# Optimization experiments

Hardware: AMD Instinct MI355X
Metric: run time of the kernel (lower is better)

The kernel has to match this reference:

```python
import jax, jax.numpy as jnp
import numpy as np
from jax import lax

B, INC1, INC2, H, W = 8, 64, 128, 128, 128
EPS = 1e-5  # BatchNorm eps; inference mode with running_mean=0, running_var=1


def leaky(x):
    return jnp.where(x >= 0, x, 0.01 * x)


def conv2d(x, w, pad=0, dil=1, groups=1):
    return lax.conv_general_dilated(
        x, w, (1, 1), [(pad, pad), (pad, pad)], rhs_dilation=(dil, dil),
        dimension_numbers=('NCHW', 'OIHW', 'NCHW'), feature_group_count=groups)


def bnlrelu(x, g, b):
    s = g / jnp.sqrt(1.0 + EPS)
    return leaky(x * s[None, :, None, None] + b[None, :, None, None])


def interp_bilinear_ac(x, oh, ow):
    # bilinear, align_corners=True (matches F.interpolate)
    ih, iw = x.shape[-2], x.shape[-1]
    ys = jnp.linspace(0.0, ih - 1.0, oh)
    xs = jnp.linspace(0.0, iw - 1.0, ow)
    y0 = jnp.floor(ys).astype(jnp.int32); y1 = jnp.minimum(y0 + 1, ih - 1)
    x0 = jnp.floor(xs).astype(jnp.int32); x1 = jnp.minimum(x0 + 1, iw - 1)
    wy = (ys - y0)[:, None]; wx = xs - x0
    rows = x[..., y0, :] * (1.0 - wy) + x[..., y1, :] * wy
    return rows[..., x0] * (1.0 - wx) + rows[..., x1] * wx


def se_layer(x, w1, w2):
    y = x.mean(axis=(2, 3))                     # [B, C]
    y = jax.nn.sigmoid(leaky(y @ w1.T) @ w2.T)  # squeeze-excite gates
    return x * y[:, :, None, None]


def dyn_multidil(f2, k):
    # per-sample depthwise conv with input-dependent 5x5 kernels, 3 dilations
    C = k.shape[1]
    def per_sample(fi, ki):
        xi = fi[None]            # [1, C, H, W]
        wi = ki[:, None, :, :]   # [C, 1, 5, 5]
        r = conv2d(xi, wi, pad=2, dil=1, groups=C)
        r = r + conv2d(xi, wi, pad=4, dil=2, groups=C)
        r = r + conv2d(xi, wi, pad=6, dil=3, groups=C)
        return r[0]
    out = jax.vmap(per_sample)(f2, k)
    return out.at[0].set(f2[0])  # original python loop starts at i=1: sample 0 untouched


def _forward(x1, k, conv1_w, conv1_g, conv1_b, conv2_w, conv2_g, conv2_b,
             conv_w, conv_bias, c0_w, c0_g, c0_b, attc_w, attc_g, attc_b,
             c05_w, c05_g, c05_b, conv0a_w, conv0a_g, conv0a_b,
             conv0b_w, conv0b_g, conv0b_b, se_w1, se_w2):
    h, w = x1.shape[2], x1.shape[3]
    kse = interp_bilinear_ac(k, h, w)                       # [B, inc1, H, W]
    va = x1.mean(axis=(2, 3), keepdims=True)                # AdaptiveAvgPool2d(1)
    bias = conv_bias[None, :, None, None]
    # MaxPool2d(1) is identity, so conv(vm) == conv(x1); bias added in both terms
    fuseadd = (conv2d(va, conv_w) + bias) + (conv2d(x1, conv_w) + bias)
    fuseadd = fuseadd * kse + fuseadd
    att = jax.nn.sigmoid(fuseadd)
    eadd = bnlrelu(conv2d(fuseadd, c0_w, pad=1), c0_g, c0_b)
    A1 = jax.nn.sigmoid(bnlrelu(conv2d(eadd, attc_w, pad=1), attc_g, attc_b))
    att = se_layer(att, se_w1, se_w2)
    f1 = bnlrelu(conv2d(x1, conv1_w), conv1_g, conv1_b)
    f2 = bnlrelu(conv2d(x1, conv2_w), conv2_g, conv2_b)
    out1 = bnlrelu(conv2d(f1, c0_w, pad=1), c0_g, c0_b)
    out1 = out1 * kse + out1
    A2 = jax.nn.sigmoid(bnlrelu(conv2d(out1, attc_w, pad=1), attc_g, attc_b))
    out2 = dyn_multidil(f2, k)
    out2 = out2 * kse + out2
    out2conv = bnlrelu(conv2d(out2, c05_w, pad=2), c05_g, c05_b)
    fuseout2 = A1 * A2 * out2conv
    finout2 = bnlrelu(conv2d(fuseout2, c05_w, pad=2), c05_g, c05_b)
    eout2 = finout2 + out2conv + f2
    out2 = bnlrelu(conv2d(eout2, c05_w, pad=2), c05_g, c05_b)
    out = jnp.concatenate([out1, out2], axis=1)             # [B, 2*inc1, H, W]
    out = bnlrelu(conv2d(out, conv0a_w), conv0a_g, conv0a_b)
    out = bnlrelu(conv2d(out, conv0b_w, pad=1), conv0b_g, conv0b_b)
    return att * out * A1


def setup_inputs() -> dict:
    key = jax.random.key(0)
    ks = jax.random.split(key, 32)
    f32 = jnp.float32
    def w(i, shape, s=0.05):
        return jax.random.normal(ks[i], shape, f32) * s
    return {
        'x1': jax.random.normal(ks[0], (B, INC2, H, W), f32),
        'k': jax.random.normal(ks[1], (B, INC1, 5, 5), f32) * 0.2,
        'conv1_w': w(2, (INC1, INC2, 1, 1)),
        'conv1_g': 1.0 + w(3, (INC1,)),
        'conv1_b': w(4, (INC1,)),
        'conv2_w': w(5, (INC1, INC2, 1, 1)),
        'conv2_g': 1.0 + w(6, (INC1,)),
        'conv2_b': w(7, (INC1,)),
        'conv_w': w(8, (INC1, INC2, 1, 1)),
        'conv_bias': w(9, (INC1,)),
        'c0_w': w(10, (INC1, INC1, 3, 3)),
        'c0_g': 1.0 + w(11, (INC1,)),
        'c0_b': w(12, (INC1,)),
        'attc_w': w(13, (INC1, INC1, 3, 3)),
        'attc_g': 1.0 + w(14, (INC1,)),
        'attc_b': w(15, (INC1,)),
        'c05_w': w(16, (INC1, INC1, 5, 5)),
        'c05_g': 1.0 + w(17, (INC1,)),
        'c05_b': w(18, (INC1,)),
        'conv0a_w': w(19, (INC1, 2 * INC1, 1, 1)),
        'conv0a_g': 1.0 + w(20, (INC1,)),
        'conv0a_b': w(21, (INC1,)),
        'conv0b_w': w(22, (INC1, INC1, 3, 3)),
        'conv0b_g': 1.0 + w(23, (INC1,)),
        'conv0b_b': w(24, (INC1,)),
        'se_w1': w(25, (INC1 // 16, INC1)),
        'se_w2': w(26, (INC1, INC1 // 16)),
    }


def reference(x1, k, conv1_w, conv1_g, conv1_b, conv2_w, conv2_g, conv2_b,
              conv_w, conv_bias, c0_w, c0_g, c0_b, attc_w, attc_g, attc_b,
              c05_w, c05_g, c05_b, conv0a_w, conv0a_g, conv0a_b,
              conv0b_w, conv0b_g, conv0b_b, se_w1, se_w2):
    return _forward(x1, k, conv1_w, conv1_g, conv1_b, conv2_w, conv2_g, conv2_b,
                    conv_w, conv_bias, c0_w, c0_g, c0_b, attc_w, attc_g, attc_b,
                    c05_w, c05_g, c05_b, conv0a_w, conv0a_g, conv0a_b,
                    conv0b_w, conv0b_g, conv0b_b, se_w1, se_w2)
```

## Files before the change

kernel.cpp:

```cpp
#include <hip/hip_runtime.h>
#include <math.h>

#define HW 16384
#define EPSC 1.00001f

typedef short bf16x8 __attribute__((ext_vector_type(8)));
typedef float f32x4 __attribute__((ext_vector_type(4)));
typedef float f32x16 __attribute__((ext_vector_type(16)));

static __device__ __forceinline__ unsigned short f2bf(float f) {
    unsigned int u = __float_as_uint(f);
    unsigned int r = (u + 0x7fffu + ((u >> 16) & 1u)) >> 16;
    return (unsigned short)r;
}
static __device__ __forceinline__ float bf2f(unsigned short u) {
    return __uint_as_float(((unsigned int)u) << 16);
}

__global__ void mean_hw_kernel(const float* __restrict__ x, float* __restrict__ out) {
    int blk = blockIdx.x;
    const float4* p4 = (const float4*)(x + (size_t)blk * HW);
    float s = 0.f;
    for (int i = threadIdx.x; i < HW / 4; i += 256) {
        float4 v = p4[i];
        s += v.x + v.y + v.z + v.w;
    }
    for (int off = 32; off > 0; off >>= 1) s += __shfl_down(s, off, 64);
    __shared__ float red[4];
    int lane = threadIdx.x & 63, wid = threadIdx.x >> 6;
    if (lane == 0) red[wid] = s;
    __syncthreads();
    if (threadIdx.x == 0)
// ... 72 lines not shown
        const float* src = x1 + ((size_t)b * 128 + h * 64) * HW + p0;
        __syncthreads();
        for (int e = threadIdx.x; e < 4096; e += 256) {
            int ci = e >> 6, px = e & 63;
            t[ci][px] = src[(size_t)ci * HW + px];
        }
        __syncthreads();
        unsigned short* dst = (h == 0 ? xa : xb) + ((size_t)b * HW + p0) * 64;
        for (int e = threadIdx.x; e < 4096; e += 256) {
            int px = e >> 6, ci = e & 63;
            dst[(size_t)px * 64 + ci] = f2bf(t[ci][px]);
        }
    }
}

__global__ void prep_w_kernel(const float* __restrict__ src, unsigned short* __restrict__ dst,
                              int CO, int CI, int K, int co_total, int co_off) {
    int idx = blockIdx.x * 256 + threadIdx.x;
    int total = CO * CI * K * K;
    if (idx >= total) return;
    int kx = idx % K, t1 = idx / K;
    int ky = t1 % K, t2 = t1 / K;
    int ci = t2 % CI, co = t2 / CI;
    int tap = ky * K + kx, chunk = ci >> 5, k32 = ci & 31;
    int kc = tap * (CI >> 5) + chunk;
    dst[((size_t)kc * co_total + co_off + co) * 32 + k32] = f2bf(src[idx]);
}

__global__ void prep_w32_kernel(const float* __restrict__ src, unsigned short* __restrict__ dst,
                                int CO, int CI, int K) {
    int idx = blockIdx.x * 256 + threadIdx.x;
    int total = CO * CI * K * K;
    if (idx >= total) return;
    int kx = idx % K, t1 = idx / K;
    int ky = t1 % K, t2 = t1 / K;
    int ci = t2 % CI, co = t2 / CI;
    int tap = ky * K + kx;
    int kstep = ci >> 4, khalf = (ci >> 3) & 1, j = ci & 7;
    int l = khalf * 32 + (co & 31), mb = co >> 5;
    dst[(((size_t)(tap * 4 + kstep) * 2 + mb) * 64 + l) * 8 + j] = f2bf(src[idx]);
}

__global__ void prep_w16_kernel(const float* __restrict__ src, unsigned short* __restrict__ dst,
                                int CO, int CI) {
    int idx = blockIdx.x * 256 + threadIdx.x;
    if (idx >= CO * CI) return;
    int ci = idx % CI, co = idx / CI;
    int ch = ci >> 5, q = (ci >> 3) & 3, j = ci & 7;
    int l = q * 16 + (co & 15), mb = co >> 4;
    dst[(((size_t)ch * 4 + mb) * 64 + l) * 8 + j] = f2bf(src[idx]);
}

template<int KSZ>
__global__ __launch_bounds__(256, 2) void conv_mfma32(
    const unsigned short* __restrict__ Xa,
    const unsigned short* __restrict__ Wp,
    const float* __restrict__ g, const float* __restrict__ bb,
    const float* __restrict__ kk,
    const unsigned short* __restrict__ eB, const unsigned short* __restrict__ eC,
    unsigned short* __restrict__ out_bf, unsigned short* __restrict__ aux_bf, int emode)
{
    constexpr int PAD = KSZ / 2;
    constexpr int TWX = 16 + 2 * PAD;
    constexpr int TWY = 16 + 2 * PAD;
    constexpr int NTAP = KSZ * KSZ;
    constexpr int WSLAB = 4 * 2 * 64 * 8;
    __shared__ unsigned short xs[TWY * TWX * 64];
    __shared__ unsigned short ws[2 * WSLAB];

    const int b = blockIdx.y;
    const int ty = (blockIdx.x >> 3) * 16, tx = (blockIdx.x & 7) * 16;
    const int tid = threadIdx.x;
    const int lane = tid & 63, wv = tid >> 6;
    const int n32 = lane & 31, khalf = lane >> 5;

    int rr[2], cc2[2];
#pragma unroll
    for (int nt = 0; nt < 2; ++nt) {
        int p = wv * 64 + nt * 32 + n32;
        rr[nt] = p >> 4; cc2[nt] = p & 15;
    }

    uint4 wst[2];
    {
        const uint4* gw = (const uint4*)Wp;
#pragma unroll
        for (int s = 0; s < 2; ++s) wst[s] = gw[tid + s * 256];
    }
    for (int e = tid; e < TWY * TWX * 8; e += 256) {
        int ci8 = e & 7, pxl = e >> 3;
        int xx = pxl % TWX, yy = pxl / TWX;
        int gy = ty + yy - PAD, gx = tx + xx - PAD;
        uint4 v = {0u, 0u, 0u, 0u};
        if (gy >= 0 && gy < 128 && gx >= 0 && gx < 128)
            v = *(const uint4*)(Xa + (((size_t)b * HW + gy * 128 + gx) * 64 + ci8 * 8));
        *(uint4*)(&xs[(size_t)pxl * 64 + ((ci8 ^ (pxl & 7)) << 3)]) = v;
    }
    {
        uint4* lw = (uint4*)ws;
#pragma unroll
        for (int s = 0; s < 2; ++s) lw[tid + s * 256] = wst[s];
    }
    __syncthreads();

    f32x16 acc[2][2];
#pragma unroll
    for (int mb = 0; mb < 2; ++mb)
#pragma unroll
        for (int nt = 0; nt < 2; ++nt)
#pragma unroll
            for (int i = 0; i < 16; ++i) acc[mb][nt][i] = 0.f;

    for (int tap = 0; tap < NTAP; ++tap) {
        if (tap + 1 < NTAP) {
            const uint4* gw = (const uint4*)Wp + (size_t)(tap + 1) * (WSLAB / 8);
#pragma unroll
            for (int s = 0; s < 2; ++s) wst[s] = gw[tid + s * 256];
        }
        const unsigned short* wl = ws + (tap & 1) * WSLAB;
        const int ky = tap / KSZ, kx = tap - ky * KSZ;
        int pxl0 = (rr[0] + ky) * TWX + cc2[0] + kx;
        int pxl1 = (rr[1] + ky) * TWX + cc2[1] + kx;
        int sw0 = (pxl0 & 7), sw1 = (pxl1 & 7);
#pragma unroll
        for (int kstep = 0; kstep < 4; ++kstep) {
            bf16x8 af0 = *(const bf16x8*)(wl + ((kstep * 2 + 0) * 64 + lane) * 8);
            bf16x8 af1 = *(const bf16x8*)(wl + ((kstep * 2 + 1) * 64 + lane) * 8);
            int gidx = kstep * 2 + khalf;
            bf16x8 b0 = *(const bf16x8*)(&xs[(size_t)pxl0 * 64 + ((gidx ^ sw0) << 3)]);
            bf16x8 b1 = *(const bf16x8*)(&xs[(size_t)pxl1 * 64 + ((gidx ^ sw1) << 3)]);
            acc[0][0] = __builtin_amdgcn_mfma_f32_32x32x16_bf16(af0, b0, acc[0][0], 0, 0, 0);
            acc[0][1] = __builtin_amdgcn_mfma_f32_32x32x16_bf16(af0, b1, acc[0][1], 0, 0, 0);
            acc[1][0] = __builtin_amdgcn_mfma_f32_32x32x16_bf16(af1, b0, acc[1][0], 0, 0, 0);
            acc[1][1] = __builtin_amdgcn_mfma_f32_32x32x16_bf16(af1, b1, acc[1][1], 0, 0, 0);
        }
        if (tap + 1 < NTAP) {
            uint4* lw = (uint4*)(ws + ((tap + 1) & 1) * WSLAB);
#pragma unroll
            for (int s = 0; s < 2; ++s) lw[tid + s * 256] = wst[s];
            __syncthreads();
        }
    }

    const float rs = rsqrtf(EPSC);
#pragma unroll
    for (int mb = 0; mb < 2; ++mb) {
#pragma unroll
        for (int nt = 0; nt < 2; ++nt) {
            const int py = ty + rr[nt];
            const int px = tx + cc2[nt];
            const size_t pix = (size_t)b * HW + py * 128 + px;
#pragma unroll
            for (int rq = 0; rq < 4; ++rq) {
                const int co0 = mb * 32 + rq * 8 + khalf * 4;
                float v4[4];
#pragma unroll
                for (int rg = 0; rg < 4; ++rg) {
                    int co = co0 + rg;
                    float v = acc[mb][nt][rq * 4 + rg];
                    v = fmaf(v, g[co] * rs, bb[co]);
                    v = v >= 0.f ? v : 0.01f * v;
                    if (emode == 1 || emode == 6) v = 1.0f / (1.0f + __expf(-v));
                    else if (emode == 2)
                        v *= (1.0f + kse_val(kk + (size_t)(b * 64 + co) * 25, py, px));
                    v4[rg] = v;
                }
                if (emode == 6) {
                    ushort4 e = *(const ushort4*)(eB + pix * 64 + co0);
                    *(ushort4*)(out_bf + pix * 64 + co0) = (ushort4){
                        f2bf(v4[0] * bf2f(e.x)), f2bf(v4[1] * bf2f(e.y)),
                        f2bf(v4[2] * bf2f(e.z)), f2bf(v4[3] * bf2f(e.w))};
                } else if (emode == 4) {
                    *(ushort4*)(out_bf + pix * 64 + co0) =
                        (ushort4){f2bf(v4[0]), f2bf(v4[1]), f2bf(v4[2]), f2bf(v4[3])};
                    ushort4 e = *(const ushort4*)(eB + pix * 64 + co0);
                    *(ushort4*)(aux_bf + pix * 64 + co0) = (ushort4){
                        f2bf(v4[0] * bf2f(e.x)), f2bf(v4[1] * bf2f(e.y)),
                        f2bf(v4[2] * bf2f(e.z)), f2bf(v4[3] * bf2f(e.w))};
                } else if (emode == 5) {
                    ushort4 e1 = *(const ushort4*)(eB + pix * 64 + co0);
                    ushort4 e2 = *(const ushort4*)(eC + pix * 64 + co0);
                    *(ushort4*)(out_bf + pix * 64 + co0) = (ushort4){
                        f2bf(v4[0] + bf2f(e1.x) + bf2f(e2.x)),
                        f2bf(v4[1] + bf2f(e1.y) + bf2f(e2.y)),
                        f2bf(v4[2] + bf2f(e1.z) + bf2f(e2.z)),
                        f2bf(v4[3] + bf2f(e1.w) + bf2f(e2.w))};
                } else {
                    *(ushort4*)(out_bf + pix * 64 + co0) =
                        (ushort4){f2bf(v4[0]), f2bf(v4[1]), f2bf(v4[2]), f2bf(v4[3])};
                }
            }
        }
    }
}

__global__ __launch_bounds__(256, 2) void conv_mfma1x1(
    const unsigned short* __restrict__ Xa, const unsigned short* __restrict__ Xb,
    const unsigned short* __restrict__ Wp,
    const float* __restrict__ g, const float* __restrict__ bb,
    unsigned short* __restrict__ out_bf)
{
    constexpr int CI = 128;
    __shared__ unsigned short xs[128 * CI];
    __shared__ unsigned short ws[4 * 4 * 64 * 8];
    const int b = blockIdx.y;
    const int ty = (blockIdx.x >> 3) * 8, tx = (blockIdx.x & 7) * 16;
    const int tid = threadIdx.x;
    const int lane = tid & 63, wv = tid >> 6;
    const int n = lane & 15, quad = lane >> 4;

    {
// ... 26 lines not shown
        for (int nt = 0; nt < 2; ++nt) {
            int pxl = (r0 + nt) * 16 + n;
            bfr[nt] = *(const bf16x8*)(&xs[(size_t)pxl * CI +
                                           (((ch * 4 + quad) ^ (pxl & 7)) << 3)]);
        }
#pragma unroll
        for (int mb = 0; mb < 4; ++mb) {
            bf16x8 af = *(const bf16x8*)(ws + ((ch * 4 + mb) * 64 + lane) * 8);
#pragma unroll
            for (int nt = 0; nt < 2; ++nt)
                acc[mb][nt] = __builtin_amdgcn_mfma_f32_16x16x32_bf16(
                    af, bfr[nt], acc[mb][nt], 0, 0, 0);
        }
    }

    const float rs = rsqrtf(EPSC);
#pragma unroll
    for (int mb = 0; mb < 4; ++mb) {
#pragma unroll
        for (int nt = 0; nt < 2; ++nt) {
            const int py = ty + r0 + nt, px = tx + n;
            const size_t pix = (size_t)b * HW + py * 128 + px;
            const int co0 = mb * 16 + quad * 4;
            float v4[4];
#pragma unroll
            for (int rg = 0; rg < 4; ++rg) {
                float v = fmaf(acc[mb][nt][rg], g[co0 + rg] * rs, bb[co0 + rg]);
                v4[rg] = v >= 0.f ? v : 0.01f * v;
            }
            *(ushort4*)(out_bf + pix * 64 + co0) =
                (ushort4){f2bf(v4[0]), f2bf(v4[1]), f2bf(v4[2]), f2bf(v4[3])};
        }
    }
}

__global__ __launch_bounds__(256, 2) void conv1x1_triple(
    const unsigned short* __restrict__ Xa, const unsigned short* __restrict__ Xb,
    const unsigned short* __restrict__ Wp,
    const float* __restrict__ cva, const float* __restrict__ cbias,
    const float* __restrict__ g1, const float* __restrict__ b1,
    const float* __restrict__ g2, const float* __restrict__ b2,
    const float* __restrict__ kk,
    unsigned short* __restrict__ fuse_bf, unsigned short* __restrict__ att0_bf,
    unsigned short* __restrict__ f1_bf,
    float* __restrict__ f2_f32, unsigned short* __restrict__ f2_bf)
{
    constexpr int CI = 128;
    __shared__ unsigned short xs[128 * CI];
    __shared__ unsigned short ws[4 * 192 * 32];
    const int b = blockIdx.y;
    const int ty = (blockIdx.x >> 3) * 8, tx = (blockIdx.x & 7) * 16;
    const int tid = threadIdx.x;
    const int lane = tid & 63, wv = tid >> 6;
    const int n = lane & 15, quad = lane >> 4;

    {
        const uint4* gw = (const uint4*)Wp;
        uint4* lw = (uint4*)ws;
#pragma unroll
        for (int s = 0; s < 12; ++s) lw[tid + s * 256] = gw[tid + s * 256];
    }
    for (int e = tid; e < 128 * 16; e += 256) {
        int ci8 = e & 15, pxl = e >> 4;
        int gy = ty + (pxl >> 4), gx = tx + (pxl & 15);
        const unsigned short* src = (ci8 >= 8) ? Xb : Xa;
        int c8 = ci8 & 7;
        uint4 v = *(const uint4*)(src + (((size_t)b * HW + gy * 128 + gx) * 64 + c8 * 8));
        *(uint4*)(&xs[(size_t)pxl * CI + ((ci8 ^ (pxl & 7)) << 3)]) = v;
    }
    __syncthreads();

    f32x4 acc[12][2];
#pragma unroll
    for (int mb = 0; mb < 12; ++mb)
#pragma unroll
        for (int nt = 0; nt < 2; ++nt) acc[mb][nt] = (f32x4){0.f, 0.f, 0.f, 0.f};

    const int r0 = wv * 2;
#pragma unroll
    for (int ch = 0; ch < 4; ++ch) {
        bf16x8 bfr[2];
#pragma unroll
        for (int nt = 0; nt < 2; ++nt) {
            int pxl = (r0 + nt) * 16 + n;
            bfr[nt] = *(const bf16x8*)(&xs[(size_t)pxl * CI +
                                           (((ch * 4 + quad) ^ (pxl & 7)) << 3)]);
        }
#pragma unroll
        for (int mb = 0; mb < 12; ++mb) {
            bf16x8 af = *(const bf16x8*)(ws + (ch * 192 + mb * 16 + n) * 32 + quad * 8);
#pragma unroll
            for (int nt = 0; nt < 2; ++nt)
                acc[mb][nt] = __builtin_amdgcn_mfma_f32_16x16x32_bf16(
                    af, bfr[nt], acc[mb][nt], 0, 0, 0);
        }
    }

    const float rs = rsqrtf(EPSC);
#pragma unroll
    for (int mb = 0; mb < 12; ++mb) {
#pragma unroll
        for (int nt = 0; nt < 2; ++nt) {
            const int py = ty + r0 + nt;
            const int px = tx + n;
            const size_t pix = (size_t)b * HW + py * 128 + px;
            const int cg = mb * 16 + quad * 4;
            if (mb < 4) {
                float v4[4], s4[4];
#pragma unroll
                for (int rg = 0; rg < 4; ++rg) {
                    int co = cg + rg;
                    float base = cva[b * 64 + co] + 2.0f * cbias[co];
                    float fa = (acc[mb][nt][rg] + base) *
                               (1.0f + kse_val(kk + (size_t)(b * 64 + co) * 25, py, px));
                    v4[rg] = fa;
                    s4[rg] = 1.0f / (1.0f + __expf(-fa));
                }
                *(ushort4*)(fuse_bf + pix * 64 + cg) =
                    (ushort4){f2bf(v4[0]), f2bf(v4[1]), f2bf(v4[2]), f2bf(v4[3])};
                *(ushort4*)(att0_bf + pix * 64 + cg) =
                    (ushort4){f2bf(s4[0]), f2bf(s4[1]), f2bf(s4[2]), f2bf(s4[3])};
            } else if (mb < 8) {
                int co0 = cg - 64;
                float v4[4];
#pragma unroll
                for (int rg = 0; rg < 4; ++rg) {
                    float v = fmaf(acc[mb][nt][rg], g1[co0 + rg] * rs, b1[co0 + rg]);
                    v4[rg] = v >= 0.f ? v : 0.01f * v;
                }
                *(ushort4*)(f1_bf + pix * 64 + co0) =
                    (ushort4){f2bf(v4[0]), f2bf(v4[1]), f2bf(v4[2]), f2bf(v4[3])};
            } else {
                int co0 = cg - 128;
                float v4[4];
#pragma unroll
                for (int rg = 0; rg < 4; ++rg) {
                    float v = fmaf(acc[mb][nt][rg], g2[co0 + rg] * rs, b2[co0 + rg]);
                    v4[rg] = v >= 0.f ? v : 0.01f * v;
                    f2_f32[(size_t)(b * 64 + co0 + rg) * HW + py * 128 + px] = v4[rg];
                }
                *(ushort4*)(f2_bf + pix * 64 + co0) =
                    (ushort4){f2bf(v4[0]), f2bf(v4[1]), f2bf(v4[2]), f2bf(v4[3])};
            }
        }
    }
}

__global__ __launch_bounds__(256) void dyndil_kernel(const float* __restrict__ f2,
                                                     const float* __restrict__ kk,
                                                     unsigned short* __restrict__ out2bf) {
    __shared__ float xl[44][148];
    int b = blockIdx.x >> 8, c = (blockIdx.x >> 2) & 63, band = blockIdx.x & 3;
    int y0 = band * 32;
    int tid = threadIdx.x;
    int r = tid >> 3, s = tid & 7;
    int x0 = s * 16;
    int y = y0 + r;
    const float* xp = f2 + (size_t)(b * 64 + c) * HW;
    const float* kt = kk + (size_t)(b * 64 + c) * 25;
    float acc[16];

    if (b != 0) {
        for (int e = tid; e < 44 * 148; e += 256) {
            int rr = e / 148, cc = e - rr * 148;
            int yy = y0 + rr - 6, xx = cc - 8;
// ... 39 lines not shown
#pragma unroll
        for (int i = 0; i < 4; i++) {
            float4 v = p4[i];
            acc[i*4] = v.x; acc[i*4+1] = v.y; acc[i*4+2] = v.z; acc[i*4+3] = v.w;
        }
    }
    float ys = y * (4.0f / 127.0f);
    int yi0 = (int)ys; if (yi0 > 4) yi0 = 4;
    int yi1 = yi0 + 1; if (yi1 > 4) yi1 = 4;
    float wy = ys - (float)yi0;
    float ry0 = kt[yi0*5+0] * (1.f-wy) + kt[yi1*5+0] * wy;
    float ry1 = kt[yi0*5+1] * (1.f-wy) + kt[yi1*5+1] * wy;
    float ry2 = kt[yi0*5+2] * (1.f-wy) + kt[yi1*5+2] * wy;
    float ry3 = kt[yi0*5+3] * (1.f-wy) + kt[yi1*5+3] * wy;
    float ry4 = kt[yi0*5+4] * (1.f-wy) + kt[yi1*5+4] * wy;
    unsigned short* op = out2bf + ((size_t)b * HW + (size_t)y * 128 + x0) * 64 + c;
#pragma unroll
    for (int e = 0; e < 16; e++) {
        int x = x0 + e;
        float xs2 = x * (4.0f / 127.0f);
        int xi0 = (int)xs2; if (xi0 > 4) xi0 = 4;
        float wx = xs2 - (float)xi0;
        float a = xi0==0 ? ry0 : xi0==1 ? ry1 : xi0==2 ? ry2 : xi0==3 ? ry3 : ry4;
        float bs = xi0>=3 ? ry4 : (xi0==2 ? ry3 : (xi0==1 ? ry2 : ry1));
        float kv = a + (bs - a) * wx;
        op[(size_t)e * 64] = f2bf(acc[e] * (1.0f + kv));
    }
}

__global__ void final_kernel(const unsigned short* __restrict__ att0,
                             const float* __restrict__ scale,
                             const unsigned short* __restrict__ outb,
                             const unsigned short* __restrict__ a1,
                             float* __restrict__ o) {
    __shared__ float t[64][65];
    int b = blockIdx.y;
    int p0 = blockIdx.x * 64;
    int tid = threadIdx.x;
    for (int e = tid; e < 4096; e += 256) {
        int px = e >> 6, c = e & 63;
        size_t idx = ((size_t)b * HW + p0 + px) * 64 + c;
// ... 38 lines not shown
    const float* se_w2 = (const float*)d_in[26];

    const size_t U = (size_t)8 * HW * 64 * 2;
    unsigned char* P = (unsigned char*)d_ws;
    unsigned short* x1a        = (unsigned short*)(P + 0 * U);
    unsigned short* x1b        = (unsigned short*)(P + 1 * U);
    unsigned short* att0_bf    = (unsigned short*)(P + 2 * U);
    unsigned short* fuse_bf    = (unsigned short*)(P + 3 * U);
    unsigned short* f1_bf      = (unsigned short*)(P + 4 * U);
    float*          f2         = (float*)         (P + 5 * U);
    unsigned short* f2_bf      = (unsigned short*)(P + 7 * U);
    unsigned short* A1_bf      = (unsigned short*)(P + 8 * U);
    unsigned short* eadd_bf    = (unsigned short*)(P + 9 * U);
    unsigned short* out1_bf    = (unsigned short*)(P + 10 * U);
    unsigned short* A12_bf     = (unsigned short*)(P + 11 * U);
    unsigned short* out2_bf     = x1a;
    unsigned short* oc_bf       = x1b;
    unsigned short* fuseout2_bf = fuse_bf;
    unsigned short* eout2_bf    = f1_bf;
    unsigned short* out2fin_bf  = eadd_bf;
    unsigned short* outb_bf     = out1_bf;
    unsigned short* outa_bf     = A12_bf;

    unsigned char* W0 = P + 12 * U;
    unsigned short* Wp1   = (unsigned short*)(W0);
    unsigned short* Wc0   = (unsigned short*)(W0 + 49152);
    unsigned short* Wattc = (unsigned short*)(W0 + 122880);
    unsigned short* Wc05  = (unsigned short*)(W0 + 196608);
    unsigned short* Wc0a  = (unsigned short*)(W0 + 401408);
    unsigned short* Wc0b  = (unsigned short*)(W0 + 417792);
    float* va   = (float*)(W0 + 491520);
    float* cva  = va + 1024;
    float* part = cva + 512;
    float* sesc = part + 8192;

    const dim3 g32(64, 8);
    const dim3 g16(128, 8);

    mean_hw_kernel<<<1024, 256, 0, stream>>>(x1, va);
    convva_kernel<<<1, 512, 0, stream>>>(va, conv_w, cva);
    repack_x1_kernel<<<dim3(256, 8), 256, 0, stream>>>(x1, x1a, x1b);
    prep_w_kernel<<<32, 256, 0, stream>>>(conv_w,   Wp1, 64, 128, 1, 192, 0);
    prep_w_kernel<<<32, 256, 0, stream>>>(conv1_w,  Wp1, 64, 128, 1, 192, 64);
    prep_w_kernel<<<32, 256, 0, stream>>>(conv2_w,  Wp1, 64, 128, 1, 192, 128);
    prep_w32_kernel<<<144, 256, 0, stream>>>(c0_w,    Wc0,   64, 64, 3);
    prep_w32_kernel<<<144, 256, 0, stream>>>(attc_w,  Wattc, 64, 64, 3);
    prep_w32_kernel<<<400, 256, 0, stream>>>(c05_w,   Wc05,  64, 64, 5);
    prep_w16_kernel<<<32, 256, 0, stream>>>(conv0a_w, Wc0a,  64, 128);
    prep_w32_kernel<<<144, 256, 0, stream>>>(conv0b_w, Wc0b, 64, 64, 3);

    conv1x1_triple<<<g16, 256, 0, stream>>>(x1a, x1b, Wp1, cva, conv_bias,
        conv1_g, conv1_b, conv2_g, conv2_b, kk, fuse_bf, att0_bf, f1_bf, f2, f2_bf);

    att_mean_part<<<dim3(16, 8), 256, 0, stream>>>(att0_bf, part);
    se_mlp_kernel<<<1, 512, 0, stream>>>(part, se_w1, se_w2, sesc);

    dyndil_kernel<<<2048, 256, 0, stream>>>(f2, kk, out2_bf);

    conv_mfma32<3><<<g32, 256, 0, stream>>>(fuse_bf, Wc0,
        c0_g, c0_b, kk, nullptr, nullptr, eadd_bf, nullptr, 0);
    conv_mfma32<3><<<g32, 256, 0, stream>>>(eadd_bf, Wattc,
        attc_g, attc_b, kk, nullptr, nullptr, A1_bf, nullptr, 1);
    conv_mfma32<3><<<g32, 256, 0, stream>>>(f1_bf, Wc0,
        c0_g, c0_b, kk, nullptr, nullptr, out1_bf, nullptr, 2);
    conv_mfma32<3><<<g32, 256, 0, stream>>>(out1_bf, Wattc,
        attc_g, attc_b, kk, A1_bf, nullptr, A12_bf, nullptr, 6);

    conv_mfma32<5><<<g32, 256, 0, stream>>>(out2_bf, Wc05,
        c05_g, c05_b, kk, A12_bf, nullptr, oc_bf, fuseout2_bf, 4);
    conv_mfma32<5><<<g32, 256, 0, stream>>>(fuseout2_bf, Wc05,
        c05_g, c05_b, kk, oc_bf, f2_bf, eout2_bf, nullptr, 5);
    conv_mfma32<5><<<g32, 256, 0, stream>>>(eout2_bf, Wc05,
        c05_g, c05_b, kk, nullptr, nullptr, out2fin_bf, nullptr, 0);

    conv_mfma1x1<<<g16, 256, 0, stream>>>(out1_bf, out2fin_bf, Wc0a,
        conv0a_g, conv0a_b, outa_bf);
    conv_mfma32<3><<<g32, 256, 0, stream>>>(outa_bf, Wc0b,
        conv0b_g, conv0b_b, kk, nullptr, nullptr, outb_bf, nullptr, 0);
    final_kernel<<<dim3(256, 8), 256, 0, stream>>>(att0_bf, sesc, outb_bf, A1_bf, (float*)d_out);
}
```

Before: 677.7 us.

## Switch convs to 16x16x32 MFMA with 8-row tiles and LDS-staged coalesced stores

The spatial conv kernels move from 32x32x16 MFMA on 16x16 tiles to 16x16x32 MFMA on 16x8 tiles, which doubles the grid and raises launch bounds to 3 blocks per CU. Epilogues now stage bf16 results through swizzled LDS and write 16-byte coalesced stores, replacing the scattered ushort4 stores. The 1x1 conv kernels are rewritten in the same style. The dyndil kernel now writes fp32 NCHW with float4 stores instead of strided bf16 writes, and a new repack kernel converts that to NHWC bf16, adding a kernel launch and extra memory traffic. Buffer aliasing is reshuffled to match.

```diff
diff --git a/kernel.cpp b/kernel.cpp
--- a/kernel.cpp
+++ b/kernel.cpp
@@ -6,7 +6,6 @@
 
 typedef short bf16x8 __attribute__((ext_vector_type(8)));
 typedef float f32x4 __attribute__((ext_vector_type(4)));
-typedef float f32x16 __attribute__((ext_vector_type(16)));
 
 static __device__ __forceinline__ unsigned short f2bf(float f) {
     unsigned int u = __float_as_uint(f);
@@ -16,6 +15,8 @@
 static __device__ __forceinline__ float bf2f(unsigned short u) {
     return __uint_as_float(((unsigned int)u) << 16);
 }
+
+union U16B { uint4 v; unsigned short s[8]; };
 
 __global__ void mean_hw_kernel(const float* __restrict__ x, float* __restrict__ out) {
     int blk = blockIdx.x;
@@ -118,45 +119,57 @@
     }
 }
 
-__global__ void prep_w_kernel(const float* __restrict__ src, unsigned short* __restrict__ dst,
-                              int CO, int CI, int K, int co_total, int co_off) {
+__global__ void repack64_kernel(const float* __restrict__ src, unsigned short* __restrict__ dst) {
+    __shared__ float t[64][65];
+    int b = blockIdx.y;
+    int p0 = blockIdx.x * 64;
+    for (int e = threadIdx.x; e < 4096; e += 256) {
+        int ci = e >> 6, px = e & 63;
+        t[ci][px] = src[((size_t)b * 64 + ci) * HW + p0 + px];
+    }
+    __syncthreads();
+    for (int e = threadIdx.x; e < 4096; e += 256) {
+        int px = e >> 6, ci = e & 63;
+        dst[((size_t)b * HW + p0 + px) * 64 + ci] = f2bf(t[ci][px]);
+    }
+}
+
+__global__ void prep_w1x1_kernel(const float* __restrict__ src, unsigned short* __restrict__ dst,
+                                 int co_off) {
     int idx = blockIdx.x * 256 + threadIdx.x;
-    int total = CO * CI * K * K;
+    if (idx >= 64 * 128) return;
+    int ci = idx % 128, co = idx / 128;
+    int ch = ci >> 5, q = (ci >> 3) & 3, j = ci & 7;
+    int gco = co_off + co;
+    int mb = gco >> 4, lane = q * 16 + (gco & 15);
+    dst[(((size_t)ch * 12 + mb) * 64 + lane) * 8 + j] = f2bf(src[idx]);
+}
+
+__global__ void prep_wtap_kernel(const float* __restrict__ src, unsigned short* __restrict__ dst,
+                                 int K) {
+    int idx = blockIdx.x * 256 + threadIdx.x;
+    int total = 64 * 64 * K * K;
     if (idx >= total) return;
     int kx = idx % K, t1 = idx / K;
     int ky = t1 % K, t2 = t1 / K;
-    int ci = t2 % CI, co = t2 / CI;
-    int tap = ky * K + kx, chunk = ci >> 5, k32 = ci & 31;
-    int kc = tap * (CI >> 5) + chunk;
-    dst[((size_t)kc * co_total + co_off + co) * 32 + k32] = f2bf(src[idx]);
-}
-
-__global__ void prep_w32_kernel(const float* __restrict__ src, unsigned short* __restrict__ dst,
-                                int CO, int CI, int K) {
+    int ci = t2 % 64, co = t2 / 64;
+    int tap = ky * K + kx;
+    int chunk = ci >> 5, q = (ci >> 3) & 3, j = ci & 7;
+    int lane = q * 16 + (co & 15), mb = (co >> 4) & 3;
+    dst[((((size_t)tap * 2 + chunk) * 4 + mb) * 64 + lane) * 8 + j] = f2bf(src[idx]);
+}
+
+__global__ void prep_w16_kernel(const float* __restrict__ src, unsigned short* __restrict__ dst) {
     int idx = blockIdx.x * 256 + threadIdx.x;
-    int total = CO * CI * K * K;
-    if (idx >= total) return;
-    int kx = idx % K, t1 = idx / K;
-    int ky = t1 % K, t2 = t1 / K;
-    int ci = t2 % CI, co = t2 / CI;
-    int tap = ky * K + kx;
-    int kstep = ci >> 4, khalf = (ci >> 3) & 1, j = ci & 7;
-    int l = khalf * 32 + (co & 31), mb = co >> 5;
-    dst[(((size_t)(tap * 4 + kstep) * 2 + mb) * 64 + l) * 8 + j] = f2bf(src[idx]);
-}
-
-__global__ void prep_w16_kernel(const float* __restrict__ src, unsigned short* __restrict__ dst,
-                                int CO, int CI) {
-    int idx = blockIdx.x * 256 + threadIdx.x;
-    if (idx >= CO * CI) return;
-    int ci = idx % CI, co = idx / CI;
+    if (idx >= 64 * 128) return;
+    int ci = idx % 128, co = idx / 128;
     int ch = ci >> 5, q = (ci >> 3) & 3, j = ci & 7;
     int l = q * 16 + (co & 15), mb = co >> 4;
     dst[(((size_t)ch * 4 + mb) * 64 + l) * 8 + j] = f2bf(src[idx]);
 }
 
 template<int KSZ>
-__global__ __launch_bounds__(256, 2) void conv_mfma32(
+__global__ __launch_bounds__(256, 3) void conv_mfma(
     const unsigned short* __restrict__ Xa,
     const unsigned short* __restrict__ Wp,
     const float* __restrict__ g, const float* __restrict__ bb,
@@ -166,24 +179,17 @@
 {
     constexpr int PAD = KSZ / 2;
     constexpr int TWX = 16 + 2 * PAD;
-    constexpr int TWY = 16 + 2 * PAD;
+    constexpr int TWY = 8 + 2 * PAD;
     constexpr int NTAP = KSZ * KSZ;
-    constexpr int WSLAB = 4 * 2 * 64 * 8;
+    constexpr int WSLAB = 4096;
     __shared__ unsigned short xs[TWY * TWX * 64];
     __shared__ unsigned short ws[2 * WSLAB];
 
     const int b = blockIdx.y;
-    const int ty = (blockIdx.x >> 3) * 16, tx = (blockIdx.x & 7) * 16;
+    const int ty = (blockIdx.x >> 3) * 8, tx = (blockIdx.x & 7) * 16;
     const int tid = threadIdx.x;
     const int lane = tid & 63, wv = tid >> 6;
-    const int n32 = lane & 31, khalf = lane >> 5;
-
-    int rr[2], cc2[2];
-#pragma unroll
-    for (int nt = 0; nt < 2; ++nt) {
-        int p = wv * 64 + nt * 32 + n32;
-        rr[nt] = p >> 4; cc2[nt] = p & 15;
-    }
+    const int n = lane & 15, quad = lane >> 4;
 
     uint4 wst[2];
     {
@@ -207,14 +213,13 @@
     }
     __syncthreads();
 
-    f32x16 acc[2][2];
-#pragma unroll
-    for (int mb = 0; mb < 2; ++mb)
-#pragma unroll
-        for (int nt = 0; nt < 2; ++nt)
-#pragma unroll
-            for (int i = 0; i < 16; ++i) acc[mb][nt][i] = 0.f;
-
+    f32x4 acc[4][2];
+#pragma unroll
+    for (int mb = 0; mb < 4; ++mb)
+#pragma unroll
+        for (int nt = 0; nt < 2; ++nt) acc[mb][nt] = (f32x4){0.f, 0.f, 0.f, 0.f};
+
+    const int r0 = wv * 2;
     for (int tap = 0; tap < NTAP; ++tap) {
         if (tap + 1 < NTAP) {
             const uint4* gw = (const uint4*)Wp + (size_t)(tap + 1) * (WSLAB / 8);
@@ -223,20 +228,25 @@
         }
         const unsigned short* wl = ws + (tap & 1) * WSLAB;
         const int ky = tap / KSZ, kx = tap - ky * KSZ;
-        int pxl0 = (rr[0] + ky) * TWX + cc2[0] + kx;
-        int pxl1 = (rr[1] + ky) * TWX + cc2[1] + kx;
-        int sw0 = (pxl0 & 7), sw1 = (pxl1 & 7);
-#pragma unroll
-        for (int kstep = 0; kstep < 4; ++kstep) {
-            bf16x8 af0 = *(const bf16x8*)(wl + ((kstep * 2 + 0) * 64 + lane) * 8);
-            bf16x8 af1 = *(const bf16x8*)(wl + ((kstep * 2 + 1) * 64 + lane) * 8);
-            int gidx = kstep * 2 + khalf;
-            bf16x8 b0 = *(const bf16x8*)(&xs[(size_t)pxl0 * 64 + ((gidx ^ sw0) << 3)]);
-            bf16x8 b1 = *(const bf16x8*)(&xs[(size_t)pxl1 * 64 + ((gidx ^ sw1) << 3)]);
-            acc[0][0] = __builtin_amdgcn_mfma_f32_32x32x16_bf16(af0, b0, acc[0][0], 0, 0, 0);
-            acc[0][1] = __builtin_amdgcn_mfma_f32_32x32x16_bf16(af0, b1, acc[0][1], 0, 0, 0);
-            acc[1][0] = __builtin_amdgcn_mfma_f32_32x32x16_bf16(af1, b0, acc[1][0], 0, 0, 0);
-            acc[1][1] = __builtin_amdgcn_mfma_f32_32x32x16_bf16(af1, b1, acc[1][1], 0, 0, 0);
+#pragma unroll
+        for (int ch = 0; ch < 2; ++ch) {
+            bf16x8 af[4];
+#pragma unroll
+            for (int mb = 0; mb < 4; ++mb)
+                af[mb] = *(const bf16x8*)(wl + ((ch * 4 + mb) * 64 + lane) * 8);
+            bf16x8 bfr[2];
+#pragma unroll
+            for (int nt = 0; nt < 2; ++nt) {
+                int pxl = (r0 + nt + ky) * TWX + n + kx;
+                bfr[nt] = *(const bf16x8*)(&xs[(size_t)pxl * 64 +
+                                               (((ch * 4 + quad) ^ (pxl & 7)) << 3)]);
+            }
+#pragma unroll
+            for (int mb = 0; mb < 4; ++mb)
+#pragma unroll
+                for (int nt = 0; nt < 2; ++nt)
+                    acc[mb][nt] = __builtin_amdgcn_mfma_f32_16x16x32_bf16(
+                        af[mb], bfr[nt], acc[mb][nt], 0, 0, 0);
         }
         if (tap + 1 < NTAP) {
             uint4* lw = (uint4*)(ws + ((tap + 1) & 1) * WSLAB);
@@ -246,59 +256,192 @@
         }
     }
 
+    __syncthreads();
+    unsigned short* stg = xs;
     const float rs = rsqrtf(EPSC);
 #pragma unroll
-    for (int mb = 0; mb < 2; ++mb) {
+    for (int mb = 0; mb < 4; ++mb) {
 #pragma unroll
         for (int nt = 0; nt < 2; ++nt) {
-            const int py = ty + rr[nt];
-            const int px = tx + cc2[nt];
-            const size_t pix = (size_t)b * HW + py * 128 + px;
-#pragma unroll
-            for (int rq = 0; rq < 4; ++rq) {
-                const int co0 = mb * 32 + rq * 8 + khalf * 4;
-                float v4[4];
-#pragma unroll
-                for (int rg = 0; rg < 4; ++rg) {
-                    int co = co0 + rg;
-                    float v = acc[mb][nt][rq * 4 + rg];
-                    v = fmaf(v, g[co] * rs, bb[co]);
+            const int pixl = (r0 + nt) * 16 + n;
+            const int py = ty + r0 + nt, px = tx + n;
+            const int co0 = mb * 16 + quad * 4;
+            float v4[4];
+#pragma unroll
+            for (int rg = 0; rg < 4; ++rg) {
+                int co = co0 + rg;
+                float v = fmaf(acc[mb][nt][rg], g[co] * rs, bb[co]);
+                v = v >= 0.f ? v : 0.01f * v;
+                if (emode == 1 || emode == 6) v = 1.0f / (1.0f + __expf(-v));
+                else if (emode == 2)
+                    v *= (1.0f + kse_val(kk + (size_t)(b * 64 + co) * 25, py, px));
+                v4[rg] = v;
+            }
+            int gq = co0 >> 3, rem = co0 & 7;
+            *(ushort4*)(stg + pixl * 64 + ((gq ^ (pixl & 7)) << 3) + rem) =
+                (ushort4){f2bf(v4[0]), f2bf(v4[1]), f2bf(v4[2]), f2bf(v4[3])};
+        }
+    }
+    __syncthreads();
+#pragma unroll
+    for (int it = 0; it < 4; ++it) {
+        int idx = it * 256 + tid;
+        int pixl = idx >> 3, s = idx & 7;
+        int cog = s ^ (pixl & 7);
+        U16B v; v.v = *(const uint4*)(stg + pixl * 64 + s * 8);
+        int py = ty + (pixl >> 4), px = tx + (pixl & 15);
+        size_t gofs = ((size_t)b * HW + py * 128 + px) * 64 + cog * 8;
+        if (emode == 6) {
+            U16B e; e.v = *(const uint4*)(eB + gofs);
+            U16B o;
+#pragma unroll
+            for (int j = 0; j < 8; ++j) o.s[j] = f2bf(bf2f(v.s[j]) * bf2f(e.s[j]));
+            *(uint4*)(out_bf + gofs) = o.v;
+        } else if (emode == 4) {
+            *(uint4*)(out_bf + gofs) = v.v;
+            U16B e; e.v = *(const uint4*)(eB + gofs);
+            U16B o;
+#pragma unroll
+            for (int j = 0; j < 8; ++j) o.s[j] = f2bf(bf2f(v.s[j]) * bf2f(e.s[j]));
+            *(uint4*)(aux_bf + gofs) = o.v;
+        } else if (emode == 5) {
+            U16B e1; e1.v = *(const uint4*)(eB + gofs);
+            U16B e2; e2.v = *(const uint4*)(eC + gofs);
+            U16B o;
+#pragma unroll
+            for (int j = 0; j < 8; ++j)
+                o.s[j] = f2bf(bf2f(v.s[j]) + bf2f(e1.s[j]) + bf2f(e2.s[j]));
+            *(uint4*)(out_bf + gofs) = o.v;
+        } else {
+            *(uint4*)(out_bf + gofs) = v.v;
+        }
+    }
+}
+
+__global__ __launch_bounds__(256, 2) void conv1x1_triple(
+    const unsigned short* __restrict__ Xa, const unsigned short* __restrict__ Xb,
+    const unsigned short* __restrict__ Wp,
+    const float* __restrict__ cva, const float* __restrict__ cbias,
+    const float* __restrict__ g1, const float* __restrict__ b1,
+    const float* __restrict__ g2, const float* __restrict__ b2,
+    const float* __restrict__ kk,
+    unsigned short* __restrict__ fuse_bf, unsigned short* __restrict__ att0_bf,
+    unsigned short* __restrict__ f1_bf,
+    float* __restrict__ f2_f32, unsigned short* __restrict__ f2_bf)
+{
+    constexpr int CI = 128;
+    __shared__ unsigned short xs[128 * CI];
+    __shared__ unsigned short ws[4 * 12 * 64 * 8];
+    const int b = blockIdx.y;
+    const int ty = (blockIdx.x >> 3) * 8, tx = (blockIdx.x & 7) * 16;
+    const int tid = threadIdx.x;
+    const int lane = tid & 63, wv = tid >> 6;
+    const int n = lane & 15, quad = lane >> 4;
+
+    {
+        const uint4* gw = (const uint4*)Wp;
+        uint4* lw = (uint4*)ws;
+#pragma unroll
+        for (int s = 0; s < 12; ++s) lw[tid + s * 256] = gw[tid + s * 256];
+    }
+    for (int e = tid; e < 128 * 16; e += 256) {
+        int ci8 = e & 15, pxl = e >> 4;
+        int gy = ty + (pxl >> 4), gx = tx + (pxl & 15);
+        const unsigned short* src = (ci8 >= 8) ? Xb : Xa;
+        int c8 = ci8 & 7;
+        uint4 v = *(const uint4*)(src + (((size_t)b * HW + gy * 128 + gx) * 64 + c8 * 8));
+        *(uint4*)(&xs[(size_t)pxl * CI + ((ci8 ^ (pxl & 7)) << 3)]) = v;
+    }
+    __syncthreads();
+
+    f32x4 acc[12][2];
+#pragma unroll
+    for (int mb = 0; mb < 12; ++mb)
+#pragma unroll
+        for (int nt = 0; nt < 2; ++nt) acc[mb][nt] = (f32x4){0.f, 0.f, 0.f, 0.f};
+
+    const int r0 = wv * 2;
+#pragma unroll
+    for (int ch = 0; ch < 4; ++ch) {
+        bf16x8 bfr[2];
+#pragma unroll
+        for (int nt = 0; nt < 2; ++nt) {
+            int pxl = (r0 + nt) * 16 + n;
+            bfr[nt] = *(const bf16x8*)(&xs[(size_t)pxl * CI +
+                                           (((ch * 4 + quad) ^ (pxl & 7)) << 3)]);
+        }
+#pragma unroll
+        for (int mb = 0; mb < 12; ++mb) {
+            bf16x8 af = *(const bf16x8*)(ws + ((ch * 12 + mb) * 64 + lane) * 8);
+#pragma unroll
+            for (int nt = 0; nt < 2; ++nt)
+                acc[mb][nt] = __builtin_amdgcn_mfma_f32_16x16x32_bf16(
+                    af, bfr[nt], acc[mb][nt], 0, 0, 0);
+        }
+    }
+
+    __syncthreads();
+    const float rs = rsqrtf(EPSC);
+#pragma unroll
+    for (int mb = 0; mb < 12; ++mb) {
+#pragma unroll
+        for (int nt = 0; nt < 2; ++nt) {
+            const int pixl = (r0 + nt) * 16 + n;
+            const int py = ty + r0 + nt, px = tx + n;
+            const int t3 = mb >> 2;
+            const int co0 = (mb & 3) * 16 + quad * 4;
+            float v4[4];
+#pragma unroll
+            for (int rg = 0; rg < 4; ++rg) {
+                int co = co0 + rg;
+                float v;
+                if (t3 == 0) {
+                    float base = cva[b * 64 + co] + 2.0f * cbias[co];
+                    v = (acc[mb][nt][rg] + base) *
+                        (1.0f + kse_val(kk + (size_t)(b * 64 + co) * 25, py, px));
+                } else if (t3 == 1) {
+                    v = fmaf(acc[mb][nt][rg], g1[co] * rs, b1[co]);
                     v = v >= 0.f ? v : 0.01f * v;
-                    if (emode == 1 || emode == 6) v = 1.0f / (1.0f + __expf(-v));
-                    else if (emode == 2)
-                        v *= (1.0f + kse_val(kk + (size_t)(b * 64 + co) * 25, py, px));
-                    v4[rg] = v;
+                } else {
+                    v = fmaf(acc[mb][nt][rg], g2[co] * rs, b2[co]);
+                    v = v >= 0.f ? v : 0.01f * v;
+                    f2_f32[(size_t)(b * 64 + co) * HW + py * 128 + px] = v;
                 }
-                if (emode == 6) {
-                    ushort4 e = *(const ushort4*)(eB + pix * 64 + co0);
-                    *(ushort4*)(out_bf + pix * 64 + co0) = (ushort4){
-                        f2bf(v4[0] * bf2f(e.x)), f2bf(v4[1] * bf2f(e.y)),
-                        f2bf(v4[2] * bf2f(e.z)), f2bf(v4[3] * bf2f(e.w))};
-                } else if (emode == 4) {
-                    *(ushort4*)(out_bf + pix * 64 + co0) =
-                        (ushort4){f2bf(v4[0]), f2bf(v4[1]), f2bf(v4[2]), f2bf(v4[3])};
-                    ushort4 e = *(const ushort4*)(eB + pix * 64 + co0);
-                    *(ushort4*)(aux_bf + pix * 64 + co0) = (ushort4){
-                        f2bf(v4[0] * bf2f(e.x)), f2bf(v4[1] * bf2f(e.y)),
-                        f2bf(v4[2] * bf2f(e.z)), f2bf(v4[3] * bf2f(e.w))};
-                } else if (emode == 5) {
-                    ushort4 e1 = *(const ushort4*)(eB + pix * 64 + co0);
-                    ushort4 e2 = *(const ushort4*)(eC + pix * 64 + co0);
-                    *(ushort4*)(out_bf + pix * 64 + co0) = (ushort4){
-                        f2bf(v4[0] + bf2f(e1.x) + bf2f(e2.x)),
-                        f2bf(v4[1] + bf2f(e1.y) + bf2f(e2.y)),
-                        f2bf(v4[2] + bf2f(e1.z) + bf2f(e2.z)),
-                        f2bf(v4[3] + bf2f(e1.w) + bf2f(e2.w))};
-                } else {
-                    *(ushort4*)(out_bf + pix * 64 + co0) =
-                        (ushort4){f2bf(v4[0]), f2bf(v4[1]), f2bf(v4[2]), f2bf(v4[3])};
-                }
+                v4[rg] = v;
             }
-        }
-    }
-}
-
-__global__ __launch_bounds__(256, 2) void conv_mfma1x1(
+            unsigned short* stg = (t3 == 2) ? xs : (ws + t3 * 8192);
+            int gq = co0 >> 3, rem = co0 & 7;
+            *(ushort4*)(stg + pixl * 64 + ((gq ^ (pixl & 7)) << 3) + rem) =
+                (ushort4){f2bf(v4[0]), f2bf(v4[1]), f2bf(v4[2]), f2bf(v4[3])};
+        }
+    }
+    __syncthreads();
+#pragma unroll
+    for (int it = 0; it < 12; ++it) {
+        int t3 = it >> 2;
+        int idx = (it & 3) * 256 + tid;
+        int pixl = idx >> 3, s = idx & 7;
+        int cog = s ^ (pixl & 7);
+        const unsigned short* stg = (t3 == 2) ? xs : (ws + t3 * 8192);
+        U16B v; v.v = *(const uint4*)(stg + pixl * 64 + s * 8);
+        int py = ty + (pixl >> 4), px = tx + (pixl & 15);
+        size_t gofs = ((size_t)b * HW + py * 128 + px) * 64 + cog * 8;
+        if (t3 == 0) {
+            *(uint4*)(fuse_bf + gofs) = v.v;
+            U16B o;
+#pragma unroll
+            for (int j = 0; j < 8; ++j)
+                o.s[j] = f2bf(1.0f / (1.0f + __expf(-bf2f(v.s[j]))));
+            *(uint4*)(att0_bf + gofs) = o.v;
+        } else if (t3 == 1) {
+            *(uint4*)(f1_bf + gofs) = v.v;
+        } else {
+            *(uint4*)(f2_bf + gofs) = v.v;
+        }
+    }
+}
+
+__global__ __launch_bounds__(256, 3) void conv_mfma1x1(
     const unsigned short* __restrict__ Xa, const unsigned short* __restrict__ Xb,
     const unsigned short* __restrict__ Wp,
     const float* __restrict__ g, const float* __restrict__ bb,
@@ -355,13 +498,13 @@
         }
     }
 
+    __syncthreads();
     const float rs = rsqrtf(EPSC);
 #pragma unroll
     for (int mb = 0; mb < 4; ++mb) {
 #pragma unroll
         for (int nt = 0; nt < 2; ++nt) {
-            const int py = ty + r0 + nt, px = tx + n;
-            const size_t pix = (size_t)b * HW + py * 128 + px;
+            const int pixl = (r0 + nt) * 16 + n;
             const int co0 = mb * 16 + quad * 4;
             float v4[4];
 #pragma unroll
@@ -369,127 +512,26 @@
                 float v = fmaf(acc[mb][nt][rg], g[co0 + rg] * rs, bb[co0 + rg]);
                 v4[rg] = v >= 0.f ? v : 0.01f * v;
             }
-            *(ushort4*)(out_bf + pix * 64 + co0) =
+            int gq = co0 >> 3, rem = co0 & 7;
+            *(ushort4*)(ws + pixl * 64 + ((gq ^ (pixl & 7)) << 3) + rem) =
                 (ushort4){f2bf(v4[0]), f2bf(v4[1]), f2bf(v4[2]), f2bf(v4[3])};
         }
     }
-}
-
-__global__ __launch_bounds__(256, 2) void conv1x1_triple(
-    const unsigned short* __restrict__ Xa, const unsigned short* __restrict__ Xb,
-    const unsigned short* __restrict__ Wp,
-    const float* __restrict__ cva, const float* __restrict__ cbias,
-    const float* __restrict__ g1, const float* __restrict__ b1,
-    const float* __restrict__ g2, const float* __restrict__ b2,
-    const float* __restrict__ kk,
-    unsigned short* __restrict__ fuse_bf, unsigned short* __restrict__ att0_bf,
-    unsigned short* __restrict__ f1_bf,
-    float* __restrict__ f2_f32, unsigned short* __restrict__ f2_bf)
-{
-    constexpr int CI = 128;
-    __shared__ unsigned short xs[128 * CI];
-    __shared__ unsigned short ws[4 * 192 * 32];
-    const int b = blockIdx.y;
-    const int ty = (blockIdx.x >> 3) * 8, tx = (blockIdx.x & 7) * 16;
-    const int tid = threadIdx.x;
-    const int lane = tid & 63, wv = tid >> 6;
-    const int n = lane & 15, quad = lane >> 4;
-
-    {
-        const uint4* gw = (const uint4*)Wp;
-        uint4* lw = (uint4*)ws;
-#pragma unroll
-        for (int s = 0; s < 12; ++s) lw[tid + s * 256] = gw[tid + s * 256];
-    }
-    for (int e = tid; e < 128 * 16; e += 256) {
-        int ci8 = e & 15, pxl = e >> 4;
-        int gy = ty + (pxl >> 4), gx = tx + (pxl & 15);
-        const unsigned short* src = (ci8 >= 8) ? Xb : Xa;
-        int c8 = ci8 & 7;
-        uint4 v = *(const uint4*)(src + (((size_t)b * HW + gy * 128 + gx) * 64 + c8 * 8));
-        *(uint4*)(&xs[(size_t)pxl * CI + ((ci8 ^ (pxl & 7)) << 3)]) = v;
-    }
-    __syncthreads();
-
-    f32x4 acc[12][2];
-#pragma unroll
-    for (int mb = 0; mb < 12; ++mb)
-#pragma unroll
-        for (int nt = 0; nt < 2; ++nt) acc[mb][nt] = (f32x4){0.f, 0.f, 0.f, 0.f};
-
-    const int r0 = wv * 2;
-#pragma unroll
-    for (int ch = 0; ch < 4; ++ch) {
-        bf16x8 bfr[2];
-#pragma unroll
-        for (int nt = 0; nt < 2; ++nt) {
-            int pxl = (r0 + nt) * 16 + n;
-            bfr[nt] = *(const bf16x8*)(&xs[(size_t)pxl * CI +
-                                           (((ch * 4 + quad) ^ (pxl & 7)) << 3)]);
-        }
-#pragma unroll
-        for (int mb = 0; mb < 12; ++mb) {
-            bf16x8 af = *(const bf16x8*)(ws + (ch * 192 + mb * 16 + n) * 32 + quad * 8);
-#pragma unroll
-            for (int nt = 0; nt < 2; ++nt)
-                acc[mb][nt] = __builtin_amdgcn_mfma_f32_16x16x32_bf16(
-                    af, bfr[nt], acc[mb][nt], 0, 0, 0);
-        }
-    }
-
-    const float rs = rsqrtf(EPSC);
-#pragma unroll
-    for (int mb = 0; mb < 12; ++mb) {
-#pragma unroll
-        for (int nt = 0; nt < 2; ++nt) {
-            const int py = ty + r0 + nt;
-            const int px = tx + n;
-            const size_t pix = (size_t)b * HW + py * 128 + px;
-            const int cg = mb * 16 + quad * 4;
-            if (mb < 4) {
-                float v4[4], s4[4];
-#pragma unroll
-                for (int rg = 0; rg < 4; ++rg) {
-                    int co = cg + rg;
-                    float base = cva[b * 64 + co] + 2.0f * cbias[co];
-                    float fa = (acc[mb][nt][rg] + base) *
-                               (1.0f + kse_val(kk + (size_t)(b * 64 + co) * 25, py, px));
-                    v4[rg] = fa;
-                    s4[rg] = 1.0f / (1.0f + __expf(-fa));
-                }
-                *(ushort4*)(fuse_bf + pix * 64 + cg) =
-                    (ushort4){f2bf(v4[0]), f2bf(v4[1]), f2bf(v4[2]), f2bf(v4[3])};
-                *(ushort4*)(att0_bf + pix * 64 + cg) =
-                    (ushort4){f2bf(s4[0]), f2bf(s4[1]), f2bf(s4[2]), f2bf(s4[3])};
-            } else if (mb < 8) {
-                int co0 = cg - 64;
-                float v4[4];
-#pragma unroll
-                for (int rg = 0; rg < 4; ++rg) {
-                    float v = fmaf(acc[mb][nt][rg], g1[co0 + rg] * rs, b1[co0 + rg]);
-                    v4[rg] = v >= 0.f ? v : 0.01f * v;
-                }
-                *(ushort4*)(f1_bf + pix * 64 + co0) =
-                    (ushort4){f2bf(v4[0]), f2bf(v4[1]), f2bf(v4[2]), f2bf(v4[3])};
-            } else {
-                int co0 = cg - 128;
-                float v4[4];
-#pragma unroll
-                for (int rg = 0; rg < 4; ++rg) {
-                    float v = fmaf(acc[mb][nt][rg], g2[co0 + rg] * rs, b2[co0 + rg]);
-                    v4[rg] = v >= 0.f ? v : 0.01f * v;
-                    f2_f32[(size_t)(b * 64 + co0 + rg) * HW + py * 128 + px] = v4[rg];
-                }
-                *(ushort4*)(f2_bf + pix * 64 + co0) =
-                    (ushort4){f2bf(v4[0]), f2bf(v4[1]), f2bf(v4[2]), f2bf(v4[3])};
-            }
-        }
+    __syncthreads();
+#pragma unroll
+    for (int it = 0; it < 4; ++it) {
+        int idx = it * 256 + tid;
+        int pixl = idx >> 3, s = idx & 7;
+        int cog = s ^ (pixl & 7);
+        uint4 v = *(const uint4*)(ws + pixl * 64 + s * 8);
+        int py = ty + (pixl >> 4), px = tx + (pixl & 15);
+        *(uint4*)(out_bf + ((size_t)b * HW + py * 128 + px) * 64 + cog * 8) = v;
     }
 }
 
 __global__ __launch_bounds__(256) void dyndil_kernel(const float* __restrict__ f2,
                                                      const float* __restrict__ kk,
-                                                     unsigned short* __restrict__ out2bf) {
+                                                     float* __restrict__ out2f) {
     __shared__ float xl[44][148];
     int b = blockIdx.x >> 8, c = (blockIdx.x >> 2) & 63, band = blockIdx.x & 3;
     int y0 = band * 32;
@@ -559,7 +601,7 @@
     float ry2 = kt[yi0*5+2] * (1.f-wy) + kt[yi1*5+2] * wy;
     float ry3 = kt[yi0*5+3] * (1.f-wy) + kt[yi1*5+3] * wy;
     float ry4 = kt[yi0*5+4] * (1.f-wy) + kt[yi1*5+4] * wy;
-    unsigned short* op = out2bf + ((size_t)b * HW + (size_t)y * 128 + x0) * 64 + c;
+    float res[16];
 #pragma unroll
     for (int e = 0; e < 16; e++) {
         int x = x0 + e;
@@ -569,7 +611,13 @@
         float a = xi0==0 ? ry0 : xi0==1 ? ry1 : xi0==2 ? ry2 : xi0==3 ? ry3 : ry4;
         float bs = xi0>=3 ? ry4 : (xi0==2 ? ry3 : (xi0==1 ? ry2 : ry1));
         float kv = a + (bs - a) * wx;
-        op[(size_t)e * 64] = f2bf(acc[e] * (1.0f + kv));
+        res[e] = acc[e] * (1.0f + kv);
+    }
+    float* op = out2f + (size_t)(b * 64 + c) * HW + (size_t)y * 128 + x0;
+#pragma unroll
+    for (int i = 0; i < 4; i++) {
+        float4 v = { res[i*4], res[i*4+1], res[i*4+2], res[i*4+3] };
+        ((float4*)op)[i] = v;
     }
 }
 
@@ -638,13 +686,14 @@
     unsigned short* eadd_bf    = (unsigned short*)(P + 9 * U);
     unsigned short* out1_bf    = (unsigned short*)(P + 10 * U);
     unsigned short* A12_bf     = (unsigned short*)(P + 11 * U);
-    unsigned short* out2_bf     = x1a;
-    unsigned short* oc_bf       = x1b;
-    unsigned short* fuseout2_bf = fuse_bf;
-    unsigned short* eout2_bf    = f1_bf;
+    float*          out2_f32    = (float*)(P + 0 * U);
+    unsigned short* out2_bf     = fuse_bf;
+    unsigned short* oc_bf       = f1_bf;
+    unsigned short* fuseout2_bf = x1a;
+    unsigned short* eout2_bf    = x1b;
     unsigned short* out2fin_bf  = eadd_bf;
-    unsigned short* outb_bf     = out1_bf;
-    unsigned short* outa_bf     = A12_bf;
+    unsigned short* outa_bf     = fuse_bf;
+    unsigned short* outb_bf     = f1_bf;
 
     unsigned char* W0 = P + 12 * U;
     unsigned short* Wp1   = (unsigned short*)(W0);
@@ -658,48 +707,49 @@
     float* part = cva + 512;
     float* sesc = part + 8192;
 
-    const dim3 g32(64, 8);
-    const dim3 g16(128, 8);
+    const dim3 gconv(128, 8);
 
     mean_hw_kernel<<<1024, 256, 0, stream>>>(x1, va);
     convva_kernel<<<1, 512, 0, stream>>>(va, conv_w, cva);
     repack_x1_kernel<<<dim3(256, 8), 256, 0, stream>>>(x1, x1a, x1b);
-    prep_w_kernel<<<32, 256, 0, stream>>>(conv_w,   Wp1, 64, 128, 1, 192, 0);
-    prep_w_kernel<<<32, 256, 0, stream>>>(conv1_w,  Wp1, 64, 128, 1, 192, 64);
-    prep_w_kernel<<<32, 256, 0, stream>>>(conv2_w,  Wp1, 64, 128, 1, 192, 128);
-    prep_w32_kernel<<<144, 256, 0, stream>>>(c0_w,    Wc0,   64, 64, 3);
-    prep_w32_kernel<<<144, 256, 0, stream>>>(attc_w,  Wattc, 64, 64, 3);
-    prep_w32_kernel<<<400, 256, 0, stream>>>(c05_w,   Wc05,  64, 64, 5);
-    prep_w16_kernel<<<32, 256, 0, stream>>>(conv0a_w, Wc0a,  64, 128);
-    prep_w32_kernel<<<144, 256, 0, stream>>>(conv0b_w, Wc0b, 64, 64, 3);
-
-    conv1x1_triple<<<g16, 256, 0, stream>>>(x1a, x1b, Wp1, cva, conv_bias,
+    prep_w1x1_kernel<<<32, 256, 0, stream>>>(conv_w,  Wp1, 0);
+    prep_w1x1_kernel<<<32, 256, 0, stream>>>(conv1_w, Wp1, 64);
+    prep_w1x1_kernel<<<32, 256, 0, stream>>>(conv2_w, Wp1, 128);
+    prep_wtap_kernel<<<144, 256, 0, stream>>>(c0_w,    Wc0,   3);
+    prep_wtap_kernel<<<144, 256, 0, stream>>>(attc_w,  Wattc, 3);
+    prep_wtap_kernel<<<400, 256, 0, stream>>>(c05_w,   Wc05,  5);
+    prep_w16_kernel<<<32, 256, 0, stream>>>(conv0a_w, Wc0a);
+    prep_wtap_kernel<<<144, 256, 0, stream>>>(conv0b_w, Wc0b, 3);
+
+    conv1x1_triple<<<gconv, 256, 0, stream>>>(x1a, x1b, Wp1, cva, conv_bias,
         conv1_g, conv1_b, conv2_g, conv2_b, kk, fuse_bf, att0_bf, f1_bf, f2, f2_bf);
 
     att_mean_part<<<dim3(16, 8), 256, 0, stream>>>(att0_bf, part);
     se_mlp_kernel<<<1, 512, 0, stream>>>(part, se_w1, se_w2, sesc);
 
-    dyndil_kernel<<<2048, 256, 0, stream>>>(f2, kk, out2_bf);
-
-    conv_mfma32<3><<<g32, 256, 0, stream>>>(fuse_bf, Wc0,
+    dyndil_kernel<<<2048, 256, 0, stream>>>(f2, kk, out2_f32);
+
+    conv_mfma<3><<<gconv, 256, 0, stream>>>(fuse_bf, Wc0,
         c0_g, c0_b, kk, nullptr, nullptr, eadd_bf, nullptr, 0);
-    conv_mfma32<3><<<g32, 256, 0, stream>>>(eadd_bf, Wattc,
+    conv_mfma<3><<<gconv, 256, 0, stream>>>(eadd_bf, Wattc,
         attc_g, attc_b, kk, nullptr, nullptr, A1_bf, nullptr, 1);
-    conv_mfma32<3><<<g32, 256, 0, stream>>>(f1_bf, Wc0,
+    conv_mfma<3><<<gconv, 256, 0, stream>>>(f1_bf, Wc0,
         c0_g, c0_b, kk, nullptr, nullptr, out1_bf, nullptr, 2);
-    conv_mfma32<3><<<g32, 256, 0, stream>>>(out1_bf, Wattc,
+    conv_mfma<3><<<gconv, 256, 0, stream>>>(out1_bf, Wattc,
         attc_g, attc_b, kk, A1_bf, nullptr, A12_bf, nullptr, 6);
 
-    conv_mfma32<5><<<g32, 256, 0, stream>>>(out2_bf, Wc05,
+    repack64_kernel<<<dim3(256, 8), 256, 0, stream>>>(out2_f32, out2_bf);
+
+    conv_mfma<5><<<gconv, 256, 0, stream>>>(out2_bf, Wc05,
         c05_g, c05_b, kk, A12_bf, nullptr, oc_bf, fuseout2_bf, 4);
-    conv_mfma32<5><<<g32, 256, 0, stream>>>(fuseout2_bf, Wc05,
+    conv_mfma<5><<<gconv, 256, 0, stream>>>(fuseout2_bf, Wc05,
         c05_g, c05_b, kk, oc_bf, f2_bf, eout2_bf, nullptr, 5);
-    conv_mfma32<5><<<g32, 256, 0, stream>>>(eout2_bf, Wc05,
+    conv_mfma<5><<<gconv, 256, 0, stream>>>(eout2_bf, Wc05,
         c05_g, c05_b, kk, nullptr, nullptr, out2fin_bf, nullptr, 0);
 
-    conv_mfma1x1<<<g16, 256, 0, stream>>>(out1_bf, out2fin_bf, Wc0a,
+    conv_mfma1x1<<<gconv, 256, 0, stream>>>(out1_bf, out2fin_bf, Wc0a,
         conv0a_g, conv0a_b, outa_bf);
-    conv_mfma32<3><<<g32, 256, 0, stream>>>(outa_bf, Wc0b,
+    conv_mfma<3><<<gconv, 256, 0, stream>>>(outa_bf, Wc0b,
         conv0b_g, conv0b_b, kk, nullptr, nullptr, outb_bf, nullptr, 0);
     final_kernel<<<dim3(256, 8), 256, 0, stream>>>(att0_bf, sesc, outb_bf, A1_bf, (float*)d_out);
 }
```

After: 577.3 us. 1.17x faster.
